# Kernel tuning notes

Hardware: AMD Instinct MI355X
Metric: run time of the kernel (lower is better)

The kernel has to match this reference:

```python
import jax, jax.numpy as jnp
import numpy as np

N_NODES = 100000


def _l2norm(v, eps=1e-12):
    return v / (jnp.linalg.norm(v) + eps)


def setup_inputs() -> dict:
    key = jax.random.key(0)
    k1, k2, k3, k4 = jax.random.split(key, 4)
    x = jax.random.normal(k1, (N_NODES, 128), dtype=jnp.float32)
    edge_index = jax.random.randint(k2, (2, 600000), 0, N_NODES, dtype=jnp.int64)
    # GCNConv weight [in, out] (xavier-ish scale), bias zeros (default init)
    W = jax.random.normal(k3, (128, 64), dtype=jnp.float32) * (1.0 / np.sqrt(128))
    bias = jnp.zeros((64,), dtype=jnp.float32)
    # learnable edge_wt initialized to ones (torch.ones_like(edge_weight))
    ew = jnp.ones((600000,), dtype=jnp.float32)
    # spectral-norm persistent power-iteration vector u (len = W.shape[0])
    u = jax.random.normal(k4, (128,), dtype=jnp.float32)
    return {"x": x, "edge_index": edge_index, "W": W, "bias": bias, "ew": ew, "u": u}


def gcn_forward(x, edge_index, W, bias, ew, u):
    N = x.shape[0]
    # --- spectral norm: one power-iteration step (u, v under stop_gradient) ---
    v = jax.lax.stop_gradient(_l2norm(W.T @ u))          # [out]
    u2 = jax.lax.stop_gradient(_l2norm(W @ v))           # [in]
    sigma = u2 @ (W @ v)
    W_sn = W / sigma
    # --- GCNConv with sigmoid edge weights, self-loops (weight 1), sym norm ---
    w = jax.nn.sigmoid(ew)                               # [E]
    row, col = edge_index[0], edge_index[1]
    deg = jax.ops.segment_sum(w, col, num_segments=N) + 1.0  # +1 from self-loop
    dis = jax.lax.rsqrt(deg)                             # deg > 0 always
    xp = x @ W_sn                                        # [N, out]
    norm_e = dis[row] * w * dis[col]                     # [E]
    msg = xp[row] * norm_e[:, None]                      # gather + scale
    agg = jax.ops.segment_sum(msg, col, num_segments=N)  # scatter-add
    out = agg + xp * (1.0 / deg)[:, None] + bias         # self-loop norm = deg^-1
    return out


def reference(x, edge_index, W, bias, ew, u):
    return gcn_forward(x, edge_index, W, bias, ew, u)
```

## Files before the change

kernel.cpp:

```cpp
#include <hip/hip_runtime.h>
#include <math.h>


#define IN_DIM 128
#define OUT_DIM 64

#define FIXSHIFT 4294967296.0
#define CNTSHIFT 40
#define DEGMASK  ((1ull << CNTSHIFT) - 1)

typedef __attribute__((ext_vector_type(4))) short s16x4;
typedef __attribute__((ext_vector_type(8))) short s16x8;
typedef __attribute__((ext_vector_type(4))) float f32x4;

__device__ __forceinline__ short f2bf(float f) {
    unsigned int u = __float_as_uint(f);
    u = u + 0x7FFFu + ((u >> 16) & 1u);
    return (short)(u >> 16);
}
__device__ __forceinline__ float bfLo(unsigned int u) {
    return __uint_as_float(u << 16);
}
__device__ __forceinline__ float bfHi(unsigned int u) {
    return __uint_as_float(u & 0xFFFF0000u);
}

__global__ __launch_bounds__(256) void edge_prep(const int* __restrict__ ei,
                                                 const float* __restrict__ ew,
                                                 unsigned long long* __restrict__ packed,
                                                 int* __restrict__ slot,
                                                 int E) {
    const int e = blockIdx.x * 256 + threadIdx.x;
    if (e >= E) return;
    const float w = 1.f / (1.f + expf(-ew[e]));
    const int col = ei[E + e];
    const unsigned long long inc =
        (1ull << CNTSHIFT) | (unsigned long long)((double)w * FIXSHIFT);
    const unsigned long long old = atomicAdd(&packed[col], inc);
    slot[e] = (int)(old >> CNTSHIFT);
}

#define APITCH 136

__global__ __launch_bounds__(256) void gemm_mfma(const float* __restrict__ x,
                                                 const float* __restrict__ W,
                                                 const unsigned long long* __restrict__ packed,
                                                 unsigned short* __restrict__ xps,
                                                 int N) {
    __shared__ short As[64 * APITCH];
    __shared__ short Wt[64 * APITCH];

    const int t = threadIdx.x;
    const int r0 = blockIdx.x * 64;

    {
        const int rl = t >> 2;
        const int q  = t & 3;
        const int grow = min(r0 + rl, N - 1);
        const float4* src = (const float4*)(x + (size_t)grow * IN_DIM + q * 32);
        short* dst = &As[rl * APITCH + q * 32];
        #pragma unroll
        for (int i = 0; i < 8; ++i) {
            const float4 v = src[i];
            s16x4 s4;
            s4.x = f2bf(v.x); s4.y = f2bf(v.y);
            s4.z = f2bf(v.z); s4.w = f2bf(v.w);
            *(s16x4*)(dst + i * 4) = s4;
        }
    }
    {
        #pragma unroll
        for (int p = 0; p < 2; ++p) {
            const int k  = p * 64 + (t >> 2);
            const int n0 = (t & 3) * 16;
            const float4* wsrc = (const float4*)(W + (size_t)k * OUT_DIM + n0);
            #pragma unroll
            for (int i = 0; i < 4; ++i) {
                const float4 v = wsrc[i];
                Wt[(n0 + 4 * i + 0) * APITCH + k] = f2bf(v.x);
                Wt[(n0 + 4 * i + 1) * APITCH + k] = f2bf(v.y);
                Wt[(n0 + 4 * i + 2) * APITCH + k] = f2bf(v.z);
                Wt[(n0 + 4 * i + 3) * APITCH + k] = f2bf(v.w);
            }
        }
    }
    __syncthreads();

    const int wave = t >> 6;
    const int lane = t & 63;
    const int m    = lane & 15;
    const int quad = lane >> 4;

    f32x4 acc[4];
    #pragma unroll
    for (int ct = 0; ct < 4; ++ct) acc[ct] = (f32x4){0.f, 0.f, 0.f, 0.f};

    const short* Abase = &As[(wave * 16 + m) * APITCH + quad * 8];
    const short* Bbase = &Wt[m * APITCH + quad * 8];

    #pragma unroll
    for (int kc = 0; kc < 4; ++kc) {
        const s16x8 a = *(const s16x8*)(Abase + kc * 32);
        #pragma unroll
        for (int ct = 0; ct < 4; ++ct) {
            const s16x8 b = *(const s16x8*)(Bbase + ct * 16 * APITCH + kc * 32);
            acc[ct] = __builtin_amdgcn_mfma_f32_16x16x32_bf16(a, b, acc[ct], 0, 0, 0);
        }
    }

    #pragma unroll
    for (int r = 0; r < 4; ++r) {
        const int grow = r0 + wave * 16 + quad * 4 + r;
        const int gc = min(grow, N - 1);
        const unsigned long long p = packed[gc];
        const float deg = (float)((double)(p & DEGMASK) * (1.0 / FIXSHIFT));
        const float dis = rsqrtf(deg + 1.f);
        if (grow < N) {
            #pragma unroll
            for (int ct = 0; ct < 4; ++ct)
                xps[(size_t)grow * OUT_DIM + ct * 16 + m] =
                    (unsigned short)f2bf(acc[ct][r] * dis);
        }
    }
}

__global__ __launch_bounds__(256) void scan_a(const unsigned long long* __restrict__ packed,
                                              int* __restrict__ pos,
                                              int* __restrict__ btot,
                                              int N) {
    __shared__ int s[256];
    const int t = threadIdx.x;
    const int i0 = blockIdx.x * 1024 + t * 4;
    int v[4]; int sum = 0;
    #pragma unroll
    for (int j = 0; j < 4; ++j) {
        unsigned long long p = (i0 + j < N) ? packed[i0 + j] : 0ull;
        v[j] = (int)(p >> CNTSHIFT);
        sum += v[j];
    }
    s[t] = sum;
    __syncthreads();
    for (int off = 1; off < 256; off <<= 1) {
        int add = (t >= off) ? s[t - off] : 0;
        __syncthreads();
        s[t] += add;
        __syncthreads();
    }
    int excl = s[t] - sum;
    #pragma unroll
    for (int j = 0; j < 4; ++j) {
        if (i0 + j < N) pos[i0 + j] = excl;
        excl += v[j];
    }
    if (t == 255) btot[blockIdx.x] = s[255];
}

__global__ __launch_bounds__(256) void scan_b_sigma(const int* __restrict__ btot,
                                                    const float* __restrict__ W,
                                                    const float* __restrict__ u,
                                                    int* __restrict__ bexcl,
                                                    float* __restrict__ inv_sigma,
                                                    int NB) {
    __shared__ int s[256];
    __shared__ float red[256];
    __shared__ float vsh[OUT_DIM];
    const int t = threadIdx.x;

    const int own = (t < NB) ? btot[t] : 0;
    s[t] = own;
    __syncthreads();
    for (int off = 1; off < 256; off <<= 1) {
        int add = (t >= off) ? s[t - off] : 0;
        __syncthreads();
        s[t] += add;
        __syncthreads();
    }
    if (t < NB) bexcl[t] = s[t] - own;

    {
        const int j = t & 63;
        const int i0 = (t >> 6) * 32;
        float tv = 0.f;
        #pragma unroll 8
        for (int i = 0; i < 32; ++i) tv += W[(i0 + i) * OUT_DIM + j] * u[i0 + i];
        red[t] = tv;
    }
    __syncthreads();
    float tvj = 0.f;
    if (t < 64) tvj = red[t] + red[t + 64] + red[t + 128] + red[t + 192];
    __syncthreads();
    red[t] = (t < 64) ? tvj * tvj : 0.f;
    __syncthreads();
    for (int sr = 128; sr > 0; sr >>= 1) {
        if (t < sr) red[t] += red[t + sr];
        __syncthreads();
    }
    const float nv = sqrtf(red[0]) + 1e-12f;
    __syncthreads();
    if (t < 64) vsh[t] = tvj / nv;
    __syncthreads();
    float wv = 0.f;
    if (t < 128) {
        #pragma unroll 8
        for (int j = 0; j < OUT_DIM; ++j) wv += W[t * OUT_DIM + j] * vsh[j];
    }
    red[t] = (t < 128) ? wv * wv : 0.f;
    __syncthreads();
    for (int sr = 128; sr > 0; sr >>= 1) {
        if (t < sr) red[t] += red[t + sr];
        __syncthreads();
    }
    if (t == 0) {
        const float s2 = red[0];
        const float sn = sqrtf(s2);
        inv_sigma[0] = (sn + 1e-12f) / s2;
    }
}

__global__ __launch_bounds__(256) void permute(const int* __restrict__ ei,
                                               const float* __restrict__ ew,
                                               const int* __restrict__ pos,
                                               const int* __restrict__ bexcl,
                                               const int* __restrict__ slot,
                                               int2* __restrict__ spk,
                                               int E) {
    const int e = blockIdx.x * 256 + threadIdx.x;
    if (e >= E) return;
    const int row = ei[e];
    const int col = ei[E + e];
    const float w = 1.f / (1.f + expf(-ew[e]));
    const int p = pos[col] + bexcl[col >> 10] + slot[e];
    int2 pk; pk.x = row; pk.y = __float_as_int(w);
    spk[p] = pk;
}

__global__ __launch_bounds__(256) void gather(const int2* __restrict__ spk,
                                              const int* __restrict__ pos,
                                              const int* __restrict__ bexcl,
                                              const unsigned long long* __restrict__ packed,
                                              const uint2* __restrict__ xps64,
                                              const float* __restrict__ bias,
                                              const float* __restrict__ inv_sigma,
                                              float* __restrict__ out,
                                              int N) {
    const int t = threadIdx.x;
    const int q  = t >> 4;
    const int ql = t & 15;
    const int n = blockIdx.x * 16 + q;
    if (n >= N) return;

    const unsigned long long p = packed[n];
    const int c = (int)(p >> CNTSHIFT);
    const float deg = (float)((double)(p & DEGMASK) * (1.0 / FIXSHIFT));
    const int st = pos[n] + bexcl[n >> 10];

    const uint2 sv = xps64[(size_t)n * 16 + ql];

    float a0 = 0.f, a1 = 0.f, a2 = 0.f, a3 = 0.f;

    for (int j0 = 0; j0 < c; j0 += 16) {
        const int rem = c - j0;
        int2 e; e.x = 0; e.y = 0;
        if (ql < rem) e = spk[st + j0 + ql];

        #pragma unroll
        for (int k = 0; k < 16; k += 4) {
            if (!__any(rem > k)) break;
            #pragma unroll
            for (int kk = 0; kk < 4; ++kk) {
                const int row = __shfl(e.x, k + kk, 16);
                const float w = __int_as_float(__shfl(e.y, k + kk, 16));
                const uint2 a = xps64[(size_t)row * 16 + ql];
                a0 += bfLo(a.x) * w;
                a1 += bfHi(a.x) * w;
                a2 += bfLo(a.y) * w;
                a3 += bfHi(a.y) * w;
            }
        }
    }

    const float isg = inv_sigma[0];
    const float sc = isg * rsqrtf(deg + 1.f);
    const float4 bv = ((const float4*)bias)[ql];
    float4 o;
    o.x = sc * (a0 + bfLo(sv.x)) + bv.x;
    o.y = sc * (a1 + bfHi(sv.x)) + bv.y;
    o.z = sc * (a2 + bfLo(sv.y)) + bv.z;
    o.w = sc * (a3 + bfHi(sv.y)) + bv.w;
    ((float4*)out)[(size_t)n * 16 + ql] = o;
}

extern "C" void kernel_launch(void* const* d_in, const int* in_sizes, int n_in,
                              void* d_out, int out_size, void* d_ws, size_t ws_size,
                              hipStream_t stream) {
    const float* x    = (const float*)d_in[0];
    const int*   ei   = (const int*)d_in[1];
    const float* W    = (const float*)d_in[2];
    const float* bias = (const float*)d_in[3];
    const float* ew   = (const float*)d_in[4];
    const float* u    = (const float*)d_in[5];
    float* out = (float*)d_out;

    const int N = in_sizes[0] / IN_DIM;
    const int E = in_sizes[4];
    const int NB = (N + 1023) / 1024;
    const int EB = (E + 255) / 256;

    char* ws = (char*)d_ws;
    size_t off = 0;
    unsigned long long* packed = (unsigned long long*)(ws + off); off += (size_t)N * 8;
    int*   slot = (int*)  (ws + off); off += (size_t)E * 4;
    int*   pos  = (int*)  (ws + off); off += (size_t)N * 4;
    int*   btot = (int*)  (ws + off); off += 4096;
    int*   bexcl= (int*)  (ws + off); off += 4096;
    float* isg  = (float*)(ws + off); off += 1024;
    int2*  spk  = (int2*) (ws + off); off += (size_t)E * 8;
    unsigned short* xps = (unsigned short*)(ws + off); off += (size_t)N * OUT_DIM * 2;

    hipMemsetAsync(packed, 0, (size_t)N * 8, stream);
    edge_prep<<<EB, 256, 0, stream>>>(ei, ew, packed, slot, E);
    gemm_mfma<<<(N + 63) / 64, 256, 0, stream>>>(x, W, packed, xps, N);
    scan_a<<<NB, 256, 0, stream>>>(packed, pos, btot, N);
    scan_b_sigma<<<1, 256, 0, stream>>>(btot, W, u, bexcl, isg, NB);
    permute<<<EB, 256, 0, stream>>>(ei, ew, pos, bexcl, slot, spk, E);
    gather<<<(N + 15) / 16, 256, 0, stream>>>(spk, pos, bexcl, packed,
                                              (const uint2*)xps, bias, isg, out, N);
}
```

Before: 178.4 us.

## Fuse all GCN stages into one cooperative persistent kernel with grid syncs

Replaces the memset plus six-kernel pipeline with a single cooperative kernel that runs degree counting, scan, spectral-norm sigma, GEMM, permutation and gather as phases separated by grid-wide syncs. Scan blocks, the sigma block and GEMM tiles run concurrently in one phase, and the block-total scan is recomputed per block in shared memory instead of in a separate launch. This is meant to remove launch overheads and inter-kernel gaps. In exchange, the grid is capped at occupancy-limited size, so the edge and gather phases become grid-stride loops, and GEMM is spread across fewer blocks. It falls back to the old path if the cooperative launch fails.

Result: slower. 421.8 us (+136.5%).

```diff
diff --git a/kernel.cpp b/kernel.cpp
--- a/kernel.cpp
+++ b/kernel.cpp
@@ -1,5 +1,8 @@
 #include <hip/hip_runtime.h>
+#include <hip/hip_cooperative_groups.h>
 #include <math.h>
+
+namespace cg = cooperative_groups;
 
 
 #define IN_DIM 128
@@ -14,15 +17,271 @@
 typedef __attribute__((ext_vector_type(4))) float f32x4;
 
 __device__ __forceinline__ short f2bf(float f) {
-    unsigned int u = __float_as_uint(f);
-    u = u + 0x7FFFu + ((u >> 16) & 1u);
-    return (short)(u >> 16);
-}
-__device__ __forceinline__ float bfLo(unsigned int u) {
-    return __uint_as_float(u << 16);
-}
-__device__ __forceinline__ float bfHi(unsigned int u) {
-    return __uint_as_float(u & 0xFFFF0000u);
+    unsigned int v = __float_as_uint(f);
+    v = v + 0x7FFFu + ((v >> 16) & 1u);
+    return (short)(v >> 16);
+}
+__device__ __forceinline__ float bfLo(unsigned int v) {
+    return __uint_as_float(v << 16);
+}
+__device__ __forceinline__ float bfHi(unsigned int v) {
+    return __uint_as_float(v & 0xFFFF0000u);
+}
+
+#define APITCH 136
+
+__global__ __launch_bounds__(256) void mega(
+    const float* __restrict__ x, const int* __restrict__ ei,
+    const float* __restrict__ W, const float* __restrict__ bias,
+    const float* __restrict__ ew, const float* __restrict__ u,
+    float* __restrict__ out,
+    unsigned long long* __restrict__ packed, int* __restrict__ slot,
+    int* __restrict__ pos, int* __restrict__ btot,
+    float* __restrict__ inv_sigma, int2* __restrict__ spk,
+    unsigned short* __restrict__ xps,
+    int N, int E, int NB)
+{
+    cg::grid_group gridg = cg::this_grid();
+
+    __shared__ __align__(16) short As[64 * APITCH];
+    __shared__ __align__(16) short Wt[64 * APITCH];
+    __shared__ int bexcl_s[128];
+
+    const int t = threadIdx.x;
+    const int bid = blockIdx.x;
+    const int G = gridDim.x;
+    const int gtid = bid * 256 + t;
+    const int gstride = G * 256;
+
+    for (int i = gtid; i < N; i += gstride) packed[i] = 0ull;
+    gridg.sync();
+
+    for (int e = gtid; e < E; e += gstride) {
+        const float w = 1.f / (1.f + expf(-ew[e]));
+        const int col = ei[E + e];
+        const unsigned long long inc =
+            (1ull << CNTSHIFT) | (unsigned long long)((double)w * FIXSHIFT);
+        const unsigned long long old = atomicAdd(&packed[col], inc);
+        slot[e] = (int)(old >> CNTSHIFT);
+    }
+    gridg.sync();
+
+    if (bid < NB) {
+        int* s = (int*)As;
+        const int i0 = bid * 1024 + t * 4;
+        int v[4]; int sum = 0;
+        #pragma unroll
+        for (int j = 0; j < 4; ++j) {
+            unsigned long long pk = (i0 + j < N) ? packed[i0 + j] : 0ull;
+            v[j] = (int)(pk >> CNTSHIFT);
+            sum += v[j];
+        }
+        s[t] = sum;
+        __syncthreads();
+        for (int off = 1; off < 256; off <<= 1) {
+            int add = (t >= off) ? s[t - off] : 0;
+            __syncthreads();
+            s[t] += add;
+            __syncthreads();
+        }
+        int excl = s[t] - sum;
+        #pragma unroll
+        for (int j = 0; j < 4; ++j) {
+            if (i0 + j < N) pos[i0 + j] = excl;
+            excl += v[j];
+        }
+        if (t == 255) btot[bid] = s[255];
+    } else if (bid == G - 1) {
+        float* red = (float*)As;
+        float* vsh = (float*)Wt;
+        {
+            const int j = t & 63;
+            const int i0 = (t >> 6) * 32;
+            float tv = 0.f;
+            #pragma unroll 8
+            for (int i = 0; i < 32; ++i) tv += W[(i0 + i) * OUT_DIM + j] * u[i0 + i];
+            red[t] = tv;
+        }
+        __syncthreads();
+        float tvj = 0.f;
+        if (t < 64) tvj = red[t] + red[t + 64] + red[t + 128] + red[t + 192];
+        __syncthreads();
+        red[t] = (t < 64) ? tvj * tvj : 0.f;
+        __syncthreads();
+        for (int sr = 128; sr > 0; sr >>= 1) {
+            if (t < sr) red[t] += red[t + sr];
+            __syncthreads();
+        }
+        const float nv = sqrtf(red[0]) + 1e-12f;
+        __syncthreads();
+        if (t < 64) vsh[t] = tvj / nv;
+        __syncthreads();
+        float wv = 0.f;
+        if (t < 128) {
+            #pragma unroll 8
+            for (int j = 0; j < OUT_DIM; ++j) wv += W[t * OUT_DIM + j] * vsh[j];
+        }
+        red[t] = (t < 128) ? wv * wv : 0.f;
+        __syncthreads();
+        for (int sr = 128; sr > 0; sr >>= 1) {
+            if (t < sr) red[t] += red[t + sr];
+            __syncthreads();
+        }
+        if (t == 0) {
+            const float s2 = red[0];
+            const float sn = sqrtf(s2);
+            inv_sigma[0] = (sn + 1e-12f) / s2;
+        }
+    } else {
+        {
+            #pragma unroll
+            for (int p = 0; p < 2; ++p) {
+                const int k  = p * 64 + (t >> 2);
+                const int n0 = (t & 3) * 16;
+                const float4* wsrc = (const float4*)(W + (size_t)k * OUT_DIM + n0);
+                #pragma unroll
+                for (int i = 0; i < 4; ++i) {
+                    const float4 v = wsrc[i];
+                    Wt[(n0 + 4 * i + 0) * APITCH + k] = f2bf(v.x);
+                    Wt[(n0 + 4 * i + 1) * APITCH + k] = f2bf(v.y);
+                    Wt[(n0 + 4 * i + 2) * APITCH + k] = f2bf(v.z);
+                    Wt[(n0 + 4 * i + 3) * APITCH + k] = f2bf(v.w);
+                }
+            }
+        }
+        const int ntile = (N + 63) >> 6;
+        const int tstride = G - 1 - NB;
+        for (int tile = bid - NB; tile < ntile; tile += tstride) {
+            const int r0 = tile * 64;
+            {
+                const int rl = t >> 2;
+                const int qk = t & 3;
+                const int grow = min(r0 + rl, N - 1);
+                const float4* src = (const float4*)(x + (size_t)grow * IN_DIM + qk * 32);
+                short* dst = &As[rl * APITCH + qk * 32];
+                #pragma unroll
+                for (int i = 0; i < 8; ++i) {
+                    const float4 v = src[i];
+                    s16x4 s4;
+                    s4.x = f2bf(v.x); s4.y = f2bf(v.y);
+                    s4.z = f2bf(v.z); s4.w = f2bf(v.w);
+                    *(s16x4*)(dst + i * 4) = s4;
+                }
+            }
+            __syncthreads();
+
+            const int wave = t >> 6;
+            const int lane = t & 63;
+            const int m    = lane & 15;
+            const int quad = lane >> 4;
+
+            f32x4 acc[4];
+            #pragma unroll
+            for (int ct = 0; ct < 4; ++ct) acc[ct] = (f32x4){0.f, 0.f, 0.f, 0.f};
+
+            const short* Abase = &As[(wave * 16 + m) * APITCH + quad * 8];
+            const short* Bbase = &Wt[m * APITCH + quad * 8];
+
+            #pragma unroll
+            for (int kc = 0; kc < 4; ++kc) {
+                const s16x8 a = *(const s16x8*)(Abase + kc * 32);
+                #pragma unroll
+                for (int ct = 0; ct < 4; ++ct) {
+                    const s16x8 b = *(const s16x8*)(Bbase + ct * 16 * APITCH + kc * 32);
+                    acc[ct] = __builtin_amdgcn_mfma_f32_16x16x32_bf16(a, b, acc[ct], 0, 0, 0);
+                }
+            }
+
+            #pragma unroll
+            for (int r = 0; r < 4; ++r) {
+                const int grow = r0 + wave * 16 + quad * 4 + r;
+                const int gc = min(grow, N - 1);
+                const unsigned long long p = packed[gc];
+                const float deg = (float)((double)(p & DEGMASK) * (1.0 / FIXSHIFT));
+                const float dis = rsqrtf(deg + 1.f);
+                if (grow < N) {
+                    #pragma unroll
+                    for (int ct = 0; ct < 4; ++ct)
+                        xps[(size_t)grow * OUT_DIM + ct * 16 + m] =
+                            (unsigned short)f2bf(acc[ct][r] * dis);
+                }
+            }
+            __syncthreads();
+        }
+    }
+    gridg.sync();
+
+    {
+        int* s = (int*)As;
+        const int own = (t < NB) ? btot[t] : 0;
+        s[t] = own;
+        __syncthreads();
+        for (int off = 1; off < 256; off <<= 1) {
+            int add = (t >= off) ? s[t - off] : 0;
+            __syncthreads();
+            s[t] += add;
+            __syncthreads();
+        }
+        if (t < NB) bexcl_s[t] = s[t] - own;
+        __syncthreads();
+    }
+    for (int e = gtid; e < E; e += gstride) {
+        const int row = ei[e];
+        const int col = ei[E + e];
+        const float w = 1.f / (1.f + expf(-ew[e]));
+        const int p = pos[col] + bexcl_s[col >> 10] + slot[e];
+        int2 pk; pk.x = row; pk.y = __float_as_int(w);
+        spk[p] = pk;
+    }
+    gridg.sync();
+
+    const float isg = inv_sigma[0];
+    const uint2* xps64 = (const uint2*)xps;
+    const int q  = t >> 4;
+    const int ql = t & 15;
+    for (int n0 = bid * 16; n0 < N; n0 += G * 16) {
+        const int n = n0 + q;
+        if (n < N) {
+            const unsigned long long p = packed[n];
+            const int c = (int)(p >> CNTSHIFT);
+            const float deg = (float)((double)(p & DEGMASK) * (1.0 / FIXSHIFT));
+            const int st = pos[n] + bexcl_s[n >> 10];
+
+            const uint2 sv = xps64[(size_t)n * 16 + ql];
+
+            float a0 = 0.f, a1 = 0.f, a2 = 0.f, a3 = 0.f;
+
+            for (int j0 = 0; j0 < c; j0 += 16) {
+                const int rem = c - j0;
+                int2 e; e.x = 0; e.y = 0;
+                if (ql < rem) e = spk[st + j0 + ql];
+
+                #pragma unroll
+                for (int k = 0; k < 16; k += 4) {
+                    if (!__any(rem > k)) break;
+                    #pragma unroll
+                    for (int kk = 0; kk < 4; ++kk) {
+                        const int row = __shfl(e.x, k + kk, 16);
+                        const float w = __int_as_float(__shfl(e.y, k + kk, 16));
+                        const uint2 a = xps64[(size_t)row * 16 + ql];
+                        a0 += bfLo(a.x) * w;
+                        a1 += bfHi(a.x) * w;
+                        a2 += bfLo(a.y) * w;
+                        a3 += bfHi(a.y) * w;
+                    }
+                }
+            }
+
+            const float sc = isg * rsqrtf(deg + 1.f);
+            const float4 bv = ((const float4*)bias)[ql];
+            float4 o;
+            o.x = sc * (a0 + bfLo(sv.x)) + bv.x;
+            o.y = sc * (a1 + bfHi(sv.x)) + bv.y;
+            o.z = sc * (a2 + bfLo(sv.y)) + bv.z;
+            o.w = sc * (a3 + bfHi(sv.y)) + bv.w;
+            ((float4*)out)[(size_t)n * 16 + ql] = o;
+        }
+    }
 }
 
 __global__ __launch_bounds__(256) void edge_prep(const int* __restrict__ ei,
@@ -40,25 +299,23 @@
     slot[e] = (int)(old >> CNTSHIFT);
 }
 
-#define APITCH 136
-
 __global__ __launch_bounds__(256) void gemm_mfma(const float* __restrict__ x,
                                                  const float* __restrict__ W,
                                                  const unsigned long long* __restrict__ packed,
                                                  unsigned short* __restrict__ xps,
                                                  int N) {
-    __shared__ short As[64 * APITCH];
-    __shared__ short Wt[64 * APITCH];
+    __shared__ __align__(16) short As[64 * APITCH];
+    __shared__ __align__(16) short Wt[64 * APITCH];
 
     const int t = threadIdx.x;
     const int r0 = blockIdx.x * 64;
 
     {
         const int rl = t >> 2;
-        const int q  = t & 3;
+        const int qk = t & 3;
         const int grow = min(r0 + rl, N - 1);
-        const float4* src = (const float4*)(x + (size_t)grow * IN_DIM + q * 32);
-        short* dst = &As[rl * APITCH + q * 32];
+        const float4* src = (const float4*)(x + (size_t)grow * IN_DIM + qk * 32);
+        short* dst = &As[rl * APITCH + qk * 32];
         #pragma unroll
         for (int i = 0; i < 8; ++i) {
             const float4 v = src[i];
@@ -301,9 +558,9 @@
     const float* u    = (const float*)d_in[5];
     float* out = (float*)d_out;
 
-    const int N = in_sizes[0] / IN_DIM;
-    const int E = in_sizes[4];
-    const int NB = (N + 1023) / 1024;
+    int N = in_sizes[0] / IN_DIM;
+    int E = in_sizes[4];
+    int NB = (N + 1023) / 1024;
     const int EB = (E + 255) / 256;
 
     char* ws = (char*)d_ws;
@@ -317,6 +574,35 @@
     int2*  spk  = (int2*) (ws + off); off += (size_t)E * 8;
     unsigned short* xps = (unsigned short*)(ws + off); off += (size_t)N * OUT_DIM * 2;
 
+    static int s_grid = 0;
+    static int s_coop = 1;
+    if (s_grid == 0) {
+        int dev = 0;
+        hipGetDevice(&dev);
+        hipDeviceProp_t prop;
+        hipGetDeviceProperties(&prop, dev);
+        int perCU = 0;
+        if (hipOccupancyMaxActiveBlocksPerMultiprocessor(&perCU, mega, 256, 0) != hipSuccess ||
+            perCU < 1) {
+            perCU = 1;
+        }
+        long g = (long)prop.multiProcessorCount * perCU;
+        if (g > 2048) g = 2048;
+        if (g < 128) { s_coop = 0; g = 128; }
+        s_grid = (int)g;
+    }
+
+    if (s_coop) {
+        void* args[] = {
+            (void*)&x, (void*)&ei, (void*)&W, (void*)&bias, (void*)&ew, (void*)&u,
+            (void*)&out, (void*)&packed, (void*)&slot, (void*)&pos, (void*)&btot,
+            (void*)&isg, (void*)&spk, (void*)&xps, (void*)&N, (void*)&E, (void*)&NB};
+        hipError_t err = hipLaunchCooperativeKernel(mega, dim3(s_grid), dim3(256),
+                                                    args, 0, stream);
+        if (err == hipSuccess) return;
+        s_coop = 0;
+    }
+
     hipMemsetAsync(packed, 0, (size_t)N * 8, stream);
     edge_prep<<<EB, 256, 0, stream>>>(ei, ew, packed, slot, E);
     gemm_mfma<<<(N + 63) / 64, 256, 0, stream>>>(x, W, packed, xps, N);
```

## Fuse scan and sigma into GEMM kernel; redundant block-scan in consumers; wider gather

Applied to the files above, without the earlier changes.

Merges the per-block degree scan and the spectral-norm sigma computation into the GEMM kernel, using extra blocks and the tail of the existing blocks, which removes two launches. The second-level scan over block totals is now recomputed redundantly in every block of permute and gather instead of running as a separate single-block kernel. The gather kernel now uses 8 lanes per node with 16-byte loads instead of 16 lanes with 8-byte loads, doubling the nodes per block. The trade-off is extra per-block scan and reduction work and barriers in permute and gather.

Result: faster. 173.1 us (-3.0%).

```diff
diff --git a/kernel.cpp b/kernel.cpp
--- a/kernel.cpp
+++ b/kernel.cpp
@@ -14,16 +14,18 @@
 typedef __attribute__((ext_vector_type(4))) float f32x4;
 
 __device__ __forceinline__ short f2bf(float f) {
-    unsigned int u = __float_as_uint(f);
-    u = u + 0x7FFFu + ((u >> 16) & 1u);
-    return (short)(u >> 16);
-}
-__device__ __forceinline__ float bfLo(unsigned int u) {
-    return __uint_as_float(u << 16);
-}
-__device__ __forceinline__ float bfHi(unsigned int u) {
-    return __uint_as_float(u & 0xFFFF0000u);
-}
+    unsigned int v = __float_as_uint(f);
+    v = v + 0x7FFFu + ((v >> 16) & 1u);
+    return (short)(v >> 16);
+}
+__device__ __forceinline__ float bfLo(unsigned int v) {
+    return __uint_as_float(v << 16);
+}
+__device__ __forceinline__ float bfHi(unsigned int v) {
+    return __uint_as_float(v & 0xFFFF0000u);
+}
+
+#define APITCH 136
 
 __global__ __launch_bounds__(256) void edge_prep(const int* __restrict__ ei,
                                                  const float* __restrict__ ew,
@@ -40,254 +42,285 @@
     slot[e] = (int)(old >> CNTSHIFT);
 }
 
-#define APITCH 136
-
-__global__ __launch_bounds__(256) void gemm_mfma(const float* __restrict__ x,
-                                                 const float* __restrict__ W,
-                                                 const unsigned long long* __restrict__ packed,
-                                                 unsigned short* __restrict__ xps,
-                                                 int N) {
-    __shared__ short As[64 * APITCH];
-    __shared__ short Wt[64 * APITCH];
+__global__ __launch_bounds__(256) void gemm_fused(const float* __restrict__ x,
+                                                  const float* __restrict__ W,
+                                                  const float* __restrict__ u,
+                                                  const unsigned long long* __restrict__ packed,
+                                                  unsigned short* __restrict__ xps,
+                                                  int* __restrict__ pos,
+                                                  int* __restrict__ btot,
+                                                  float* __restrict__ inv_sigma,
+                                                  int N, int NB) {
+    __shared__ __align__(16) short As[64 * APITCH];
+    __shared__ __align__(16) short Wt[64 * APITCH];
 
     const int t = threadIdx.x;
-    const int r0 = blockIdx.x * 64;
-
-    {
-        const int rl = t >> 2;
-        const int q  = t & 3;
-        const int grow = min(r0 + rl, N - 1);
-        const float4* src = (const float4*)(x + (size_t)grow * IN_DIM + q * 32);
-        short* dst = &As[rl * APITCH + q * 32];
-        #pragma unroll
-        for (int i = 0; i < 8; ++i) {
-            const float4 v = src[i];
-            s16x4 s4;
-            s4.x = f2bf(v.x); s4.y = f2bf(v.y);
-            s4.z = f2bf(v.z); s4.w = f2bf(v.w);
-            *(s16x4*)(dst + i * 4) = s4;
-        }
-    }
-    {
-        #pragma unroll
-        for (int p = 0; p < 2; ++p) {
-            const int k  = p * 64 + (t >> 2);
-            const int n0 = (t & 3) * 16;
-            const float4* wsrc = (const float4*)(W + (size_t)k * OUT_DIM + n0);
+    const int bid = blockIdx.x;
+    const int ntile = (N + 63) >> 6;
+
+    if (bid < ntile) {
+        const int r0 = bid * 64;
+        {
+            const int rl = t >> 2;
+            const int qk = t & 3;
+            const int grow = min(r0 + rl, N - 1);
+            const float4* src = (const float4*)(x + (size_t)grow * IN_DIM + qk * 32);
+            short* dst = &As[rl * APITCH + qk * 32];
             #pragma unroll
-            for (int i = 0; i < 4; ++i) {
-                const float4 v = wsrc[i];
-                Wt[(n0 + 4 * i + 0) * APITCH + k] = f2bf(v.x);
-                Wt[(n0 + 4 * i + 1) * APITCH + k] = f2bf(v.y);
-                Wt[(n0 + 4 * i + 2) * APITCH + k] = f2bf(v.z);
-                Wt[(n0 + 4 * i + 3) * APITCH + k] = f2bf(v.w);
-            }
-        }
-    }
-    __syncthreads();
-
-    const int wave = t >> 6;
-    const int lane = t & 63;
-    const int m    = lane & 15;
-    const int quad = lane >> 4;
-
-    f32x4 acc[4];
-    #pragma unroll
-    for (int ct = 0; ct < 4; ++ct) acc[ct] = (f32x4){0.f, 0.f, 0.f, 0.f};
-
-    const short* Abase = &As[(wave * 16 + m) * APITCH + quad * 8];
-    const short* Bbase = &Wt[m * APITCH + quad * 8];
-
-    #pragma unroll
-    for (int kc = 0; kc < 4; ++kc) {
-        const s16x8 a = *(const s16x8*)(Abase + kc * 32);
-        #pragma unroll
-        for (int ct = 0; ct < 4; ++ct) {
-            const s16x8 b = *(const s16x8*)(Bbase + ct * 16 * APITCH + kc * 32);
-            acc[ct] = __builtin_amdgcn_mfma_f32_16x16x32_bf16(a, b, acc[ct], 0, 0, 0);
-        }
-    }
-
-    #pragma unroll
-    for (int r = 0; r < 4; ++r) {
-        const int grow = r0 + wave * 16 + quad * 4 + r;
-        const int gc = min(grow, N - 1);
-        const unsigned long long p = packed[gc];
-        const float deg = (float)((double)(p & DEGMASK) * (1.0 / FIXSHIFT));
-        const float dis = rsqrtf(deg + 1.f);
-        if (grow < N) {
+            for (int i = 0; i < 8; ++i) {
+                const float4 v = src[i];
+                s16x4 s4;
+                s4.x = f2bf(v.x); s4.y = f2bf(v.y);
+                s4.z = f2bf(v.z); s4.w = f2bf(v.w);
+                *(s16x4*)(dst + i * 4) = s4;
+            }
+        }
+        {
             #pragma unroll
-            for (int ct = 0; ct < 4; ++ct)
-                xps[(size_t)grow * OUT_DIM + ct * 16 + m] =
-                    (unsigned short)f2bf(acc[ct][r] * dis);
-        }
-    }
-}
-
-__global__ __launch_bounds__(256) void scan_a(const unsigned long long* __restrict__ packed,
-                                              int* __restrict__ pos,
-                                              int* __restrict__ btot,
-                                              int N) {
-    __shared__ int s[256];
-    const int t = threadIdx.x;
-    const int i0 = blockIdx.x * 1024 + t * 4;
-    int v[4]; int sum = 0;
-    #pragma unroll
-    for (int j = 0; j < 4; ++j) {
-        unsigned long long p = (i0 + j < N) ? packed[i0 + j] : 0ull;
-        v[j] = (int)(p >> CNTSHIFT);
-        sum += v[j];
-    }
-    s[t] = sum;
-    __syncthreads();
-    for (int off = 1; off < 256; off <<= 1) {
-        int add = (t >= off) ? s[t - off] : 0;
-        __syncthreads();
-        s[t] += add;
-        __syncthreads();
-    }
-    int excl = s[t] - sum;
-    #pragma unroll
-    for (int j = 0; j < 4; ++j) {
-        if (i0 + j < N) pos[i0 + j] = excl;
-        excl += v[j];
-    }
-    if (t == 255) btot[blockIdx.x] = s[255];
-}
-
-__global__ __launch_bounds__(256) void scan_b_sigma(const int* __restrict__ btot,
-                                                    const float* __restrict__ W,
-                                                    const float* __restrict__ u,
-                                                    int* __restrict__ bexcl,
-                                                    float* __restrict__ inv_sigma,
-                                                    int NB) {
-    __shared__ int s[256];
-    __shared__ float red[256];
-    __shared__ float vsh[OUT_DIM];
-    const int t = threadIdx.x;
-
-    const int own = (t < NB) ? btot[t] : 0;
-    s[t] = own;
-    __syncthreads();
-    for (int off = 1; off < 256; off <<= 1) {
-        int add = (t >= off) ? s[t - off] : 0;
-        __syncthreads();
-        s[t] += add;
-        __syncthreads();
-    }
-    if (t < NB) bexcl[t] = s[t] - own;
-
-    {
-        const int j = t & 63;
-        const int i0 = (t >> 6) * 32;
-        float tv = 0.f;
-        #pragma unroll 8
-        for (int i = 0; i < 32; ++i) tv += W[(i0 + i) * OUT_DIM + j] * u[i0 + i];
-        red[t] = tv;
-    }
-    __syncthreads();
-    float tvj = 0.f;
-    if (t < 64) tvj = red[t] + red[t + 64] + red[t + 128] + red[t + 192];
-    __syncthreads();
-    red[t] = (t < 64) ? tvj * tvj : 0.f;
-    __syncthreads();
-    for (int sr = 128; sr > 0; sr >>= 1) {
-        if (t < sr) red[t] += red[t + sr];
-        __syncthreads();
-    }
-    const float nv = sqrtf(red[0]) + 1e-12f;
-    __syncthreads();
-    if (t < 64) vsh[t] = tvj / nv;
-    __syncthreads();
-    float wv = 0.f;
-    if (t < 128) {
-        #pragma unroll 8
-        for (int j = 0; j < OUT_DIM; ++j) wv += W[t * OUT_DIM + j] * vsh[j];
-    }
-    red[t] = (t < 128) ? wv * wv : 0.f;
-    __syncthreads();
-    for (int sr = 128; sr > 0; sr >>= 1) {
-        if (t < sr) red[t] += red[t + sr];
-        __syncthreads();
-    }
-    if (t == 0) {
-        const float s2 = red[0];
-        const float sn = sqrtf(s2);
-        inv_sigma[0] = (sn + 1e-12f) / s2;
+            for (int p = 0; p < 2; ++p) {
+                const int k  = p * 64 + (t >> 2);
+                const int n0 = (t & 3) * 16;
+                const float4* wsrc = (const float4*)(W + (size_t)k * OUT_DIM + n0);
+                #pragma unroll
+                for (int i = 0; i < 4; ++i) {
+                    const float4 v = wsrc[i];
+                    Wt[(n0 + 4 * i + 0) * APITCH + k] = f2bf(v.x);
+                    Wt[(n0 + 4 * i + 1) * APITCH + k] = f2bf(v.y);
+                    Wt[(n0 + 4 * i + 2) * APITCH + k] = f2bf(v.z);
+                    Wt[(n0 + 4 * i + 3) * APITCH + k] = f2bf(v.w);
+                }
+            }
+        }
+        __syncthreads();
+
+        const int wave = t >> 6;
+        const int lane = t & 63;
+        const int m    = lane & 15;
+        const int quad = lane >> 4;
+
+        f32x4 acc[4];
+        #pragma unroll
+        for (int ct = 0; ct < 4; ++ct) acc[ct] = (f32x4){0.f, 0.f, 0.f, 0.f};
+
+        const short* Abase = &As[(wave * 16 + m) * APITCH + quad * 8];
+        const short* Bbase = &Wt[m * APITCH + quad * 8];
+
+        #pragma unroll
+        for (int kc = 0; kc < 4; ++kc) {
+            const s16x8 a = *(const s16x8*)(Abase + kc * 32);
+            #pragma unroll
+            for (int ct = 0; ct < 4; ++ct) {
+                const s16x8 b = *(const s16x8*)(Bbase + ct * 16 * APITCH + kc * 32);
+                acc[ct] = __builtin_amdgcn_mfma_f32_16x16x32_bf16(a, b, acc[ct], 0, 0, 0);
+            }
+        }
+
+        #pragma unroll
+        for (int r = 0; r < 4; ++r) {
+            const int grow = r0 + wave * 16 + quad * 4 + r;
+            const int gc = min(grow, N - 1);
+            const unsigned long long p = packed[gc];
+            const float deg = (float)((double)(p & DEGMASK) * (1.0 / FIXSHIFT));
+            const float dis = rsqrtf(deg + 1.f);
+            if (grow < N) {
+                #pragma unroll
+                for (int ct = 0; ct < 4; ++ct)
+                    xps[(size_t)grow * OUT_DIM + ct * 16 + m] =
+                        (unsigned short)f2bf(acc[ct][r] * dis);
+            }
+        }
+    }
+
+    if (bid < NB) {
+        __syncthreads();
+        int* s = (int*)As;
+        const int i0 = bid * 1024 + t * 4;
+        int v[4]; int sum = 0;
+        #pragma unroll
+        for (int j = 0; j < 4; ++j) {
+            unsigned long long pk = (i0 + j < N) ? packed[i0 + j] : 0ull;
+            v[j] = (int)(pk >> CNTSHIFT);
+            sum += v[j];
+        }
+        s[t] = sum;
+        __syncthreads();
+        for (int off = 1; off < 256; off <<= 1) {
+            int add = (t >= off) ? s[t - off] : 0;
+            __syncthreads();
+            s[t] += add;
+            __syncthreads();
+        }
+        int excl = s[t] - sum;
+        #pragma unroll
+        for (int j = 0; j < 4; ++j) {
+            if (i0 + j < N) pos[i0 + j] = excl;
+            excl += v[j];
+        }
+        if (t == 255) btot[bid] = s[255];
+    } else if (bid == NB) {
+        __syncthreads();
+        float* red = (float*)As;
+        float* vsh = (float*)Wt;
+        {
+            const int j = t & 63;
+            const int i0 = (t >> 6) * 32;
+            float tv = 0.f;
+            #pragma unroll 8
+            for (int i = 0; i < 32; ++i) tv += W[(i0 + i) * OUT_DIM + j] * u[i0 + i];
+            red[t] = tv;
+        }
+        __syncthreads();
+        float tvj = 0.f;
+        if (t < 64) tvj = red[t] + red[t + 64] + red[t + 128] + red[t + 192];
+        __syncthreads();
+        red[t] = (t < 64) ? tvj * tvj : 0.f;
+        __syncthreads();
+        for (int sr = 128; sr > 0; sr >>= 1) {
+            if (t < sr) red[t] += red[t + sr];
+            __syncthreads();
+        }
+        const float nv = sqrtf(red[0]) + 1e-12f;
+        __syncthreads();
+        if (t < 64) vsh[t] = tvj / nv;
+        __syncthreads();
+        float wv = 0.f;
+        if (t < 128) {
+            #pragma unroll 8
+            for (int j = 0; j < OUT_DIM; ++j) wv += W[t * OUT_DIM + j] * vsh[j];
+        }
+        red[t] = (t < 128) ? wv * wv : 0.f;
+        __syncthreads();
+        for (int sr = 128; sr > 0; sr >>= 1) {
+            if (t < sr) red[t] += red[t + sr];
+            __syncthreads();
+        }
+        if (t == 0) {
+            const float s2 = red[0];
+            const float sn = sqrtf(s2);
+            inv_sigma[0] = (sn + 1e-12f) / s2;
+        }
     }
 }
 
 __global__ __launch_bounds__(256) void permute(const int* __restrict__ ei,
                                                const float* __restrict__ ew,
                                                const int* __restrict__ pos,
-                                               const int* __restrict__ bexcl,
+                                               const int* __restrict__ btot,
                                                const int* __restrict__ slot,
                                                int2* __restrict__ spk,
-                                               int E) {
-    const int e = blockIdx.x * 256 + threadIdx.x;
+                                               int E, int NB) {
+    __shared__ int sb[128];
+    __shared__ int bex[128];
+    const int t = threadIdx.x;
+
+    int own = 0;
+    if (t < 128) {
+        own = (t < NB) ? btot[t] : 0;
+        sb[t] = own;
+    }
+    __syncthreads();
+    for (int off = 1; off < 128; off <<= 1) {
+        int add = 0;
+        if (t < 128 && t >= off) add = sb[t - off];
+        __syncthreads();
+        if (t < 128) sb[t] += add;
+        __syncthreads();
+    }
+    if (t < 128) bex[t] = sb[t] - own;
+    __syncthreads();
+
+    const int e = blockIdx.x * 256 + t;
     if (e >= E) return;
     const int row = ei[e];
     const int col = ei[E + e];
     const float w = 1.f / (1.f + expf(-ew[e]));
-    const int p = pos[col] + bexcl[col >> 10] + slot[e];
+    const int p = pos[col] + bex[col >> 10] + slot[e];
     int2 pk; pk.x = row; pk.y = __float_as_int(w);
     spk[p] = pk;
 }
 
 __global__ __launch_bounds__(256) void gather(const int2* __restrict__ spk,
                                               const int* __restrict__ pos,
-                                              const int* __restrict__ bexcl,
+                                              const int* __restrict__ btot,
                                               const unsigned long long* __restrict__ packed,
-                                              const uint2* __restrict__ xps64,
+                                              const uint4* __restrict__ xps128,
                                               const float* __restrict__ bias,
                                               const float* __restrict__ inv_sigma,
                                               float* __restrict__ out,
-                                              int N) {
+                                              int N, int NB) {
+    __shared__ int rr[128];
     const int t = threadIdx.x;
-    const int q  = t >> 4;
-    const int ql = t & 15;
-    const int n = blockIdx.x * 16 + q;
+    const int q  = t >> 3;
+    const int el = t & 7;
+    const int n = blockIdx.x * 32 + q;
+
+    unsigned long long p = 0ull;
+    int posn = 0;
+    uint4 sv = {0u, 0u, 0u, 0u};
+    if (n < N) {
+        p = packed[n];
+        posn = pos[n];
+        sv = xps128[(size_t)n * 8 + el];
+    }
+    const float isg = inv_sigma[0];
+
+    const int K = (blockIdx.x * 32) >> 10;
+    if (t < 128) rr[t] = (t < K) ? btot[t] : 0;
+    __syncthreads();
+    for (int sr = 64; sr > 0; sr >>= 1) {
+        if (t < sr) rr[t] += rr[t + sr];
+        __syncthreads();
+    }
+    const int bsum = rr[0];
+
     if (n >= N) return;
 
-    const unsigned long long p = packed[n];
     const int c = (int)(p >> CNTSHIFT);
     const float deg = (float)((double)(p & DEGMASK) * (1.0 / FIXSHIFT));
-    const int st = pos[n] + bexcl[n >> 10];
-
-    const uint2 sv = xps64[(size_t)n * 16 + ql];
+    const int st = posn + bsum;
 
     float a0 = 0.f, a1 = 0.f, a2 = 0.f, a3 = 0.f;
-
-    for (int j0 = 0; j0 < c; j0 += 16) {
+    float a4 = 0.f, a5 = 0.f, a6 = 0.f, a7 = 0.f;
+
+    for (int j0 = 0; j0 < c; j0 += 8) {
         const int rem = c - j0;
         int2 e; e.x = 0; e.y = 0;
-        if (ql < rem) e = spk[st + j0 + ql];
-
-        #pragma unroll
-        for (int k = 0; k < 16; k += 4) {
+        if (el < rem) e = spk[st + j0 + el];
+
+        #pragma unroll
+        for (int k = 0; k < 8; k += 4) {
             if (!__any(rem > k)) break;
             #pragma unroll
             for (int kk = 0; kk < 4; ++kk) {
-                const int row = __shfl(e.x, k + kk, 16);
-                const float w = __int_as_float(__shfl(e.y, k + kk, 16));
-                const uint2 a = xps64[(size_t)row * 16 + ql];
+                const int row = __shfl(e.x, k + kk, 8);
+                const float w = __int_as_float(__shfl(e.y, k + kk, 8));
+                const uint4 a = xps128[(size_t)row * 8 + el];
                 a0 += bfLo(a.x) * w;
                 a1 += bfHi(a.x) * w;
                 a2 += bfLo(a.y) * w;
                 a3 += bfHi(a.y) * w;
-            }
-        }
-    }
-
-    const float isg = inv_sigma[0];
+                a4 += bfLo(a.z) * w;
+                a5 += bfHi(a.z) * w;
+                a6 += bfLo(a.w) * w;
+                a7 += bfHi(a.w) * w;
+            }
+        }
+    }
+
     const float sc = isg * rsqrtf(deg + 1.f);
-    const float4 bv = ((const float4*)bias)[ql];
-    float4 o;
-    o.x = sc * (a0 + bfLo(sv.x)) + bv.x;
-    o.y = sc * (a1 + bfHi(sv.x)) + bv.y;
-    o.z = sc * (a2 + bfLo(sv.y)) + bv.z;
-    o.w = sc * (a3 + bfHi(sv.y)) + bv.w;
-    ((float4*)out)[(size_t)n * 16 + ql] = o;
+    const float4 bv0 = ((const float4*)bias)[el * 2];
+    const float4 bv1 = ((const float4*)bias)[el * 2 + 1];
+    float4 o0, o1;
+    o0.x = sc * (a0 + bfLo(sv.x)) + bv0.x;
+    o0.y = sc * (a1 + bfHi(sv.x)) + bv0.y;
+    o0.z = sc * (a2 + bfLo(sv.y)) + bv0.z;
+    o0.w = sc * (a3 + bfHi(sv.y)) + bv0.w;
+    o1.x = sc * (a4 + bfLo(sv.z)) + bv1.x;
+    o1.y = sc * (a5 + bfHi(sv.z)) + bv1.y;
+    o1.z = sc * (a6 + bfLo(sv.w)) + bv1.z;
+    o1.w = sc * (a7 + bfHi(sv.w)) + bv1.w;
+    ((float4*)out)[(size_t)n * 16 + el * 2] = o0;
+    ((float4*)out)[(size_t)n * 16 + el * 2 + 1] = o1;
 }
 
 extern "C" void kernel_launch(void* const* d_in, const int* in_sizes, int n_in,
@@ -312,17 +345,17 @@
     int*   slot = (int*)  (ws + off); off += (size_t)E * 4;
     int*   pos  = (int*)  (ws + off); off += (size_t)N * 4;
     int*   btot = (int*)  (ws + off); off += 4096;
-    int*   bexcl= (int*)  (ws + off); off += 4096;
     float* isg  = (float*)(ws + off); off += 1024;
     int2*  spk  = (int2*) (ws + off); off += (size_t)E * 8;
     unsigned short* xps = (unsigned short*)(ws + off); off += (size_t)N * OUT_DIM * 2;
 
+    const int ntile = (N + 63) / 64;
+    const int g2 = (ntile > NB + 1) ? ntile : NB + 1;
+
     hipMemsetAsync(packed, 0, (size_t)N * 8, stream);
     edge_prep<<<EB, 256, 0, stream>>>(ei, ew, packed, slot, E);
-    gemm_mfma<<<(N + 63) / 64, 256, 0, stream>>>(x, W, packed, xps, N);
-    scan_a<<<NB, 256, 0, stream>>>(packed, pos, btot, N);
-    scan_b_sigma<<<1, 256, 0, stream>>>(btot, W, u, bexcl, isg, NB);
-    permute<<<EB, 256, 0, stream>>>(ei, ew, pos, bexcl, slot, spk, E);
-    gather<<<(N + 15) / 16, 256, 0, stream>>>(spk, pos, bexcl, packed,
-                                              (const uint2*)xps, bias, isg, out, N);
-}
+    gemm_fused<<<g2, 256, 0, stream>>>(x, W, u, packed, xps, pos, btot, isg, N, NB);
+    permute<<<EB, 256, 0, stream>>>(ei, ew, pos, btot, slot, spk, E, NB);
+    gather<<<(N + 31) / 32, 256, 0, stream>>>(spk, pos, btot, packed,
+                                              (const uint4*)xps, bias, isg, out, N, NB);
+}
```
